# Kernel tuning notes

Hardware: AMD Instinct MI355X
Metric: run time of the kernel (lower is better)

Reference implementation:

```python
import jax, jax.numpy as jnp
import numpy as np

B, D, H, A, P, T = 65536, 256, 4, 32, 8, 32
TAU_MIN, TAU_MAX = 0.1, 5.0


def _ln(x, g, b, eps=1e-5):
    mu = jnp.mean(x, axis=-1, keepdims=True)
    v = jnp.mean((x - mu) ** 2, axis=-1, keepdims=True)
    return (x - mu) * jax.lax.rsqrt(v + eps) * g + b


def _bn(x, g, b, m, v, eps=1e-5):
    # eval-mode BatchNorm1d using running stats
    return (x - m) * jax.lax.rsqrt(v + eps) * g + b


def setup_inputs() -> dict:
    key = jax.random.key(0)
    ks = iter(jax.random.split(key, 64))
    rn = lambda shape, s: jax.random.normal(next(ks), shape, jnp.float32) * s
    un = lambda shape: jax.random.uniform(next(ks), shape, jnp.float32, 0.5, 1.5)
    z = lambda *shape: jnp.zeros(shape, jnp.float32)
    o = lambda *shape: jnp.ones(shape, jnp.float32)
    inp = {
        'x': jax.random.normal(next(ks), (B, D), jnp.float32),
        # input BatchNorm (eval mode)
        'bn0_g': o(D), 'bn0_b': z(D), 'bn0_m': rn((D,), 0.1), 'bn0_v': un((D,)),
        # per-head EDT params, stacked over H heads
        'qw': rn((H, D, A), 0.05), 'qb': z(H, A),
        'pk': rn((H, P, A), 0.02), 'pv': rn((H, P, A), 0.02),
        'tw1': rn((H, 1, T), 0.5), 'tb1': z(H, T),
        'tw2': rn((H, T, 1), 0.5), 'tb2': z(H, 1),
        'ow': rn((H, A, A), 0.1), 'ob': z(H, A),
        'lng': o(H, A), 'lnb': z(H, A),
        # head fusion
        'fp_w': rn((H * A, D), 0.05), 'fp_b': z(D),
        'fln_g': o(D), 'fln_b': z(D),
        # SE block
        'se_w1': rn((D, D // 4), 0.05), 'se_b1': z(D // 4),
        'se_w2': rn((D // 4, D), 0.05), 'se_b2': z(D),
        # hidden block 1: 256->256 (identity residual)
        'b1_w': rn((256, 256), 0.05), 'b1_b': z(256),
        'b1_g': o(256), 'b1_bb': z(256), 'b1_m': rn((256,), 0.1), 'b1_v': un((256,)),
        # hidden block 2: 256->128
        'b2_w': rn((256, 128), 0.05), 'b2_b': z(128),
        'b2_g': o(128), 'b2_bb': z(128), 'b2_m': rn((128,), 0.1), 'b2_v': un((128,)),
        'r2_w': rn((256, 128), 0.05), 'r2_b': z(128),
        # hidden block 3: 128->64
        'b3_w': rn((128, 64), 0.05), 'b3_b': z(64),
        'b3_g': o(64), 'b3_bb': z(64), 'b3_m': rn((64,), 0.1), 'b3_v': un((64,)),
        'r3_w': rn((128, 64), 0.05), 'r3_b': z(64),
        # classifier head
        'c1_w': rn((64, 32), 0.1), 'c1_b': z(32),
        'c2_w': rn((32, 1), 0.1), 'c2_b': z(1),
    }
    return inp


def reference(x, bn0_g, bn0_b, bn0_m, bn0_v, qw, qb, pk, pv, tw1, tb1, tw2, tb2,
              ow, ob, lng, lnb, fp_w, fp_b, fln_g, fln_b, se_w1, se_b1, se_w2, se_b2,
              b1_w, b1_b, b1_g, b1_bb, b1_m, b1_v,
              b2_w, b2_b, b2_g, b2_bb, b2_m, b2_v, r2_w, r2_b,
              b3_w, b3_b, b3_g, b3_bb, b3_m, b3_v, r3_w, r3_b,
              c1_w, c1_b, c2_w, c2_b):
    gelu = lambda t: jax.nn.gelu(t, approximate=False)
    xb = _bn(x, bn0_g, bn0_b, bn0_m, bn0_v)                      # (B, D)
    # ---- multi-head EDT prototype attention (vectorized over heads) ----
    q = jnp.einsum('bi,hia->bha', xb, qw) + qb                   # (B, H, A)
    logits = jnp.einsum('bha,hpa->bhp', q, pk) / jnp.sqrt(jnp.float32(A))
    lp = jax.nn.log_softmax(logits, axis=-1)                     # pass 1: entropy
    ent = -jnp.sum(jnp.exp(lp) * lp, axis=-1) / jnp.log(jnp.float32(P))  # (B, H)
    hid = jax.nn.relu(ent[..., None] * tw1[:, 0, :] + tb1)       # (B, H, T)
    tau = TAU_MIN + (TAU_MAX - TAU_MIN) * jax.nn.sigmoid(
        jnp.einsum('bht,ht->bh', hid, tw2[:, :, 0]) + tb2[:, 0])  # (B, H)
    attn = jax.nn.softmax(logits / tau[..., None], axis=-1)      # pass 2: tempered
    ho = jnp.einsum('bhp,hpa->bha', attn, pv)
    ho = jnp.einsum('bha,hae->bhe', ho, ow) + ob
    ho = _ln(ho, lng, lnb)                                       # per-head LayerNorm
    comb = ho.reshape(ho.shape[0], H * A)                        # concat heads
    att = _ln(comb @ fp_w + fp_b + xb, fln_g, fln_b)             # fuse + residual
    # ---- SE gating ----
    se = jax.nn.sigmoid(jax.nn.relu(att @ se_w1 + se_b1) @ se_w2 + se_b2)
    h = att * se
    # ---- residual MLP stack (Dropout inactive at eval) ----
    h = gelu(_bn(h @ b1_w + b1_b, b1_g, b1_bb, b1_m, b1_v)) + h
    h = gelu(_bn(h @ b2_w + b2_b, b2_g, b2_bb, b2_m, b2_v)) + (h @ r2_w + r2_b)
    h = gelu(_bn(h @ b3_w + b3_b, b3_g, b3_bb, b3_m, b3_v)) + (h @ r3_w + r3_b)
    # ---- classifier head ----
    return jax.nn.sigmoid(gelu(h @ c1_w + c1_b) @ c2_w + c2_b)   # (B, 1)
```

## Files before the change

### kernel.cpp

```cpp
#include <hip/hip_runtime.h>
#include <math.h>


typedef unsigned short u16;
typedef __attribute__((ext_vector_type(8))) short short8;
typedef __attribute__((ext_vector_type(4))) short short4v;
typedef __attribute__((ext_vector_type(4))) float f32x4;

struct Ptrs { const float* p[51]; };

__device__ __host__ __forceinline__ u16 f2bf(float f) {
  union { float f; unsigned int i; } v; v.f = f;
  unsigned int u = v.i;
  unsigned int r = (u + 0x7fffu + ((u >> 16) & 1u)) >> 16;
  return (u16)r;
}
__device__ __forceinline__ float bf2f(u16 u) {
  union { unsigned int i; float f; } v; v.i = ((unsigned int)u) << 16; return v.f;
}
__device__ __forceinline__ float gelu_exact(float y) {
  return 0.5f * y * (1.f + erff(y * 0.70710678118654752f));
}
__device__ __forceinline__ float sigmoidf_(float y) {
  return 1.f / (1.f + expf(-y));
}

#define QWT_O   0
#define FPT_O   32768
#define SE1T_O  65536
#define SE2T_O  81920
#define B1T_O   98304
#define B2T_O   163840
#define R2T_O   196608
#define B3T_O   229376
#define R3T_O   237568
#define C1T_O   245760
#define W_TOTAL 247808
#define WSP_F_OFF 123904
#define BN0S_P 0
#define BN0T_P 256
#define PK_P   512
#define PV_P   1536
#define OW_P   2560
#define TW1_P  6656
#define TB1_P  6784
#define TW2_P  6912
#define TB2_P  7040
#define OB_P   7044
#define LNG_P  7172
#define LNB_P  7300
#define QB_P   7428
#define FPB_P  7556
#define FLNG_P 7812
#define FLNB_P 8068
#define SEB1_P 8324
#define SEB2_P 8388
#define B1S_P  8644
#define B1TT_P 8900
#define B2S_P  9156
#define B2TT_P 9284
#define R2B_P  9412
#define B3S_P  9540
#define B3TT_P 9604
#define R3B_P  9668
#define C1B_P  9732
#define C2W_P  9764
#define C2B_P  9796
#define P_TOTAL 9797

#define XSTRIDE 264

__global__ void prep_weights(Ptrs P, u16* __restrict__ w) {
  for (int idx = blockIdx.x * blockDim.x + threadIdx.x; idx < W_TOTAL;
       idx += gridDim.x * blockDim.x) {
    int i = idx; float v;
    if (i < 32768)       { int n = i >> 8, k = i & 255; v = P.p[5][(n >> 5) * 8192 + k * 32 + (n & 31)]; }
    else if (i < 65536)  { i -= 32768;  int n = i >> 7, k = i & 127; v = P.p[17][k * 256 + n]; }
    else if (i < 81920)  { i -= 65536;  int n = i >> 8, k = i & 255; v = P.p[21][k * 64 + n]; }
    else if (i < 98304)  { i -= 81920;  int n = i >> 6, k = i & 63;  v = P.p[23][k * 256 + n]; }
    else if (i < 163840) { i -= 98304;  int n = i >> 8, k = i & 255; v = P.p[25][k * 256 + n]; }
    else if (i < 196608) { i -= 163840; int n = i >> 8, k = i & 255; v = P.p[31][k * 128 + n]; }
    else if (i < 229376) { i -= 196608; int n = i >> 8, k = i & 255; v = P.p[37][k * 128 + n]; }
    else if (i < 237568) { i -= 229376; int n = i >> 7, k = i & 127; v = P.p[39][k * 64 + n]; }
    else if (i < 245760) { i -= 237568; int n = i >> 7, k = i & 127; v = P.p[45][k * 64 + n]; }
    else                 { i -= 245760; int n = i >> 6, k = i & 63;  v = P.p[47][k * 32 + n]; }
    w[idx] = f2bf(v);
  }
}

__global__ void prep_params(Ptrs P, float* __restrict__ wp) {
  int idx = blockIdx.x * blockDim.x + threadIdx.x;
  if (idx >= P_TOTAL) return;
  const float eps = 1e-5f;
  int i = idx; float v;
  if (i < 256)        { v = P.p[1][i] * rsqrtf(P.p[4][i] + eps); }
  else if (i < 512)   { int c = i - 256; float s = P.p[1][c] * rsqrtf(P.p[4][c] + eps); v = P.p[2][c] - P.p[3][c] * s; }
  else if (i < 1536)  v = P.p[7][i - 512];
  else if (i < 2560)  v = P.p[8][i - 1536];
  else if (i < 6656)  v = P.p[13][i - 2560];
  else if (i < 6784)  v = P.p[9][i - 6656];
  else if (i < 6912)  v = P.p[10][i - 6784];
  else if (i < 7040)  v = P.p[11][i - 6912];
  else if (i < 7044)  v = P.p[12][i - 7040];
  else if (i < 7172)  v = P.p[14][i - 7044];
  else if (i < 7300)  v = P.p[15][i - 7172];
  else if (i < 7428)  v = P.p[16][i - 7300];
  else if (i < 7556)  v = P.p[6][i - 7428];
  else if (i < 7812)  v = P.p[18][i - 7556];
  else if (i < 8068)  v = P.p[19][i - 7812];
  else if (i < 8324)  v = P.p[20][i - 8068];
  else if (i < 8388)  v = P.p[22][i - 8324];
  else if (i < 8644)  v = P.p[24][i - 8388];
  else if (i < 8900)  { int c = i - 8644; v = P.p[27][c] * rsqrtf(P.p[30][c] + eps); }
  else if (i < 9156)  { int c = i - 8900; float s = P.p[27][c] * rsqrtf(P.p[30][c] + eps); v = P.p[28][c] + (P.p[26][c] - P.p[29][c]) * s; }
  else if (i < 9284)  { int c = i - 9156; v = P.p[33][c] * rsqrtf(P.p[36][c] + eps); }
  else if (i < 9412)  { int c = i - 9284; float s = P.p[33][c] * rsqrtf(P.p[36][c] + eps); v = P.p[34][c] + (P.p[32][c] - P.p[35][c]) * s; }
  else if (i < 9540)  v = P.p[38][i - 9412];
  else if (i < 9604)  { int c = i - 9540; v = P.p[41][c] * rsqrtf(P.p[44][c] + eps); }
  else if (i < 9668)  { int c = i - 9604; float s = P.p[41][c] * rsqrtf(P.p[44][c] + eps); v = P.p[42][c] + (P.p[40][c] - P.p[43][c]) * s; }
  else if (i < 9732)  v = P.p[46][i - 9668];
  else if (i < 9764)  v = P.p[48][i - 9732];
  else if (i < 9796)  v = P.p[49][i - 9764];
  else                v = P.p[50][0];
  wp[idx] = v;
}

template<int K, int NT>
__device__ __forceinline__ void gemm_tile(const u16* A, const u16* __restrict__ WT,
                                          int n0, int kg, int l15, f32x4 acc[4][NT]) {
#pragma unroll
  for (int kc = 0; kc < K / 32; ++kc) {
    short8 b[NT];
#pragma unroll
    for (int nt = 0; nt < NT; ++nt)
      b[nt] = *reinterpret_cast<const short8*>(WT + (n0 + nt * 16 + l15) * K + kc * 32 + kg * 8);
#pragma unroll
    for (int m = 0; m < 4; ++m) {
      short8 a = *reinterpret_cast<const short8*>(A + (m * 16 + l15) * XSTRIDE + kc * 32 + kg * 8);
#pragma unroll
      for (int nt = 0; nt < NT; ++nt)
        acc[m][nt] = __builtin_amdgcn_mfma_f32_16x16x32_bf16(a, b[nt], acc[m][nt], 0, 0, 0);
    }
  }
}

#define ZERO_ACC(acc, NT)                                         \
  _Pragma("unroll") for (int m_ = 0; m_ < 4; ++m_)                \
  _Pragma("unroll") for (int n_ = 0; n_ < NT; ++n_)               \
    acc[m_][n_] = (f32x4){0.f, 0.f, 0.f, 0.f};

__global__ __launch_bounds__(256) void fused_kernel(const float* __restrict__ x,
                                                    const u16* __restrict__ W,
                                                    const float* __restrict__ Pg,
                                                    float* __restrict__ out) {
  __shared__ __align__(16) u16 XA[64 * XSTRIDE];
  __shared__ __align__(16) u16 XB[64 * XSTRIDE];
  __shared__ __align__(16) float PRM[9800];

  const int tid = threadIdx.x;
  const int row0 = blockIdx.x * 64;
  const int wv = tid >> 6, lane = tid & 63;
  const int kg = lane >> 4, l15 = lane & 15;

  {
    const float4* src = reinterpret_cast<const float4*>(Pg);
    float4* dst = reinterpret_cast<float4*>(PRM);
    for (int i = tid; i < 2450; i += 256) dst[i] = src[i];
  }
  {
    const float4* x4 = reinterpret_cast<const float4*>(x);
    const float4* s4 = reinterpret_cast<const float4*>(Pg + BN0S_P);
    const float4* t4 = reinterpret_cast<const float4*>(Pg + BN0T_P);
    for (int it = tid; it < 4096; it += 256) {
      int r = it >> 6, c4 = it & 63;
      float4 v = x4[(size_t)(row0 + r) * 64 + c4];
      float4 s = s4[c4];
      float4 t = t4[c4];
      short4v o;
      o[0] = (short)f2bf(v.x * s.x + t.x);
      o[1] = (short)f2bf(v.y * s.y + t.y);
      o[2] = (short)f2bf(v.z * s.z + t.z);
      o[3] = (short)f2bf(v.w * s.w + t.w);
      *reinterpret_cast<short4v*>(&XA[r * XSTRIDE + c4 * 4]) = o;
    }
  }
  __syncthreads();

  {
    f32x4 acc[4][2];
    ZERO_ACC(acc, 2)
    gemm_tile<256, 2>(XA, W + QWT_O, wv * 32, kg, l15, acc);
#pragma unroll
    for (int m = 0; m < 4; ++m)
#pragma unroll
      for (int nt = 0; nt < 2; ++nt)
#pragma unroll
        for (int i = 0; i < 4; ++i) {
          int col = wv * 32 + nt * 16 + l15;
          int row = m * 16 + kg * 4 + i;
          XB[row * XSTRIDE + col] = f2bf(acc[m][nt][i] + PRM[QB_P + col]);
        }
  }
  __syncthreads();

  {
    const int h = wv;
    const int r = lane;
    float qv[32];
#pragma unroll
    for (int j = 0; j < 4; ++j) {
      short8 s = *reinterpret_cast<const short8*>(&XB[r * XSTRIDE + h * 32 + j * 8]);
#pragma unroll
      for (int e = 0; e < 8; ++e) qv[j * 8 + e] = bf2f((u16)s[e]);
    }
    float lp[8];
#pragma unroll
    for (int p = 0; p < 8; ++p) {
      float a = 0.f;
#pragma unroll
      for (int aa = 0; aa < 32; ++aa) a += qv[aa] * PRM[PK_P + h * 256 + p * 32 + aa];
      lp[p] = a * 0.17677669529663687f;
    }
    float mx = lp[0];
#pragma unroll
    for (int p = 1; p < 8; ++p) mx = fmaxf(mx, lp[p]);
    float se = 0.f;
#pragma unroll
    for (int p = 0; p < 8; ++p) se += expf(lp[p] - mx);
    float lse = mx + logf(se);
    float ent = 0.f;
#pragma unroll
    for (int p = 0; p < 8; ++p) { float t = lp[p] - lse; ent += expf(t) * t; }
    ent = -ent * 0.48089834696298783f;
    float sacc = 0.f;
#pragma unroll
    for (int t = 0; t < 32; ++t) {
      float hd = fmaxf(ent * PRM[TW1_P + h * 32 + t] + PRM[TB1_P + h * 32 + t], 0.f);
      sacc += hd * PRM[TW2_P + h * 32 + t];
    }
    float tau = 0.1f + 4.9f * sigmoidf_(sacc + PRM[TB2_P + h]);
    float itau = 1.f / tau;
    float at[8]; float s2 = 0.f;
#pragma unroll
    for (int p = 0; p < 8; ++p) { at[p] = expf((lp[p] - mx) * itau); s2 += at[p]; }
    float is2 = 1.f / s2;
    float ho[32];
#pragma unroll
    for (int aa = 0; aa < 32; ++aa) {
      float a = 0.f;
#pragma unroll
      for (int p = 0; p < 8; ++p) a += at[p] * PRM[PV_P + h * 256 + p * 32 + aa];
      ho[aa] = a * is2;
    }
    float h2[32]; float mu = 0.f;
#pragma unroll
    for (int e = 0; e < 32; ++e) {
      float a = PRM[OB_P + h * 32 + e];
#pragma unroll
      for (int aa = 0; aa < 32; ++aa) a += ho[aa] * PRM[OW_P + h * 1024 + aa * 32 + e];
      h2[e] = a; mu += a;
    }
    mu *= 0.03125f;
    float var = 0.f;
#pragma unroll
    for (int e = 0; e < 32; ++e) { float d = h2[e] - mu; var += d * d; }
    var *= 0.03125f;
    float rs = rsqrtf(var + 1e-5f);
#pragma unroll
    for (int e = 0; e < 32; ++e) {
      float v = (h2[e] - mu) * rs * PRM[LNG_P + h * 32 + e] + PRM[LNB_P + h * 32 + e];
      XB[r * XSTRIDE + h * 32 + e] = f2bf(v);
    }
  }
  __syncthreads();

  {
    f32x4 acc[4][4];
    ZERO_ACC(acc, 4)
    gemm_tile<128, 4>(XB, W + FPT_O, wv * 64, kg, l15, acc);
#pragma unroll
    for (int m = 0; m < 4; ++m)
#pragma unroll
      for (int nt = 0; nt < 4; ++nt)
#pragma unroll
        for (int i = 0; i < 4; ++i) {
          int col = wv * 64 + nt * 16 + l15;
          int row = m * 16 + kg * 4 + i;
          float v = acc[m][nt][i] + PRM[FPB_P + col] + bf2f(XA[row * XSTRIDE + col]);
          XA[row * XSTRIDE + col] = f2bf(v);
        }
  }
  __syncthreads();
  {
    int r = tid >> 2, qd = tid & 3;
    int base = r * XSTRIDE + qd * 64;
    float s = 0.f, s2 = 0.f;
#pragma unroll
    for (int j = 0; j < 8; ++j) {
      short8 v = *reinterpret_cast<const short8*>(&XA[base + j * 8]);
#pragma unroll
      for (int e = 0; e < 8; ++e) { float f = bf2f((u16)v[e]); s += f; s2 += f * f; }
    }
    s += __shfl_xor(s, 1);  s += __shfl_xor(s, 2);
    s2 += __shfl_xor(s2, 1); s2 += __shfl_xor(s2, 2);
    float mu = s * (1.f / 256.f);
    float var = s2 * (1.f / 256.f) - mu * mu;
    float rs = rsqrtf(var + 1e-5f);
#pragma unroll
    for (int j = 0; j < 8; ++j) {
      short8 v = *reinterpret_cast<const short8*>(&XA[base + j * 8]);
      short8 o;
#pragma unroll
      for (int e = 0; e < 8; ++e) {
        int col = qd * 64 + j * 8 + e;
        float f = (bf2f((u16)v[e]) - mu) * rs * PRM[FLNG_P + col] + PRM[FLNB_P + col];
        o[e] = (short)f2bf(f);
      }
      *reinterpret_cast<short8*>(&XA[base + j * 8]) = o;
    }
  }
  __syncthreads();

  {
    f32x4 acc[4][1];
    ZERO_ACC(acc, 1)
    gemm_tile<256, 1>(XA, W + SE1T_O, wv * 16, kg, l15, acc);
#pragma unroll
    for (int m = 0; m < 4; ++m)
#pragma unroll
      for (int i = 0; i < 4; ++i) {
        int col = wv * 16 + l15;
        int row = m * 16 + kg * 4 + i;
        XB[row * XSTRIDE + col] = f2bf(fmaxf(acc[m][0][i] + PRM[SEB1_P + col], 0.f));
      }
  }
  __syncthreads();

  {
    f32x4 acc[4][4];
    ZERO_ACC(acc, 4)
    gemm_tile<64, 4>(XB, W + SE2T_O, wv * 64, kg, l15, acc);
#pragma unroll
    for (int m = 0; m < 4; ++m)
#pragma unroll
      for (int nt = 0; nt < 4; ++nt)
#pragma unroll
        for (int i = 0; i < 4; ++i) {
          int col = wv * 64 + nt * 16 + l15;
          int row = m * 16 + kg * 4 + i;
          float g = sigmoidf_(acc[m][nt][i] + PRM[SEB2_P + col]);
          float a = bf2f(XA[row * XSTRIDE + col]);
          XA[row * XSTRIDE + col] = f2bf(a * g);
        }
  }
  __syncthreads();

  {
    f32x4 acc[4][4];
    ZERO_ACC(acc, 4)
    gemm_tile<256, 4>(XA, W + B1T_O, wv * 64, kg, l15, acc);
#pragma unroll
    for (int m = 0; m < 4; ++m)
#pragma unroll
      for (int nt = 0; nt < 4; ++nt)
#pragma unroll
        for (int i = 0; i < 4; ++i) {
          int col = wv * 64 + nt * 16 + l15;
          int row = m * 16 + kg * 4 + i;
          float y = PRM[B1S_P + col] * acc[m][nt][i] + PRM[B1TT_P + col];
          float g = gelu_exact(y);
          float h0 = bf2f(XA[row * XSTRIDE + col]);
          XB[row * XSTRIDE + col] = f2bf(g + h0);
        }
  }
  __syncthreads();

  {
    f32x4 acc[4][2], accr[4][2];
    ZERO_ACC(acc, 2)
    ZERO_ACC(accr, 2)
    gemm_tile<256, 2>(XB, W + B2T_O, wv * 32, kg, l15, acc);
    gemm_tile<256, 2>(XB, W + R2T_O, wv * 32, kg, l15, accr);
#pragma unroll
    for (int m = 0; m < 4; ++m)
#pragma unroll
      for (int nt = 0; nt < 2; ++nt)
#pragma unroll
        for (int i = 0; i < 4; ++i) {
          int col = wv * 32 + nt * 16 + l15;
          int row = m * 16 + kg * 4 + i;
          float y = PRM[B2S_P + col] * acc[m][nt][i] + PRM[B2TT_P + col];
          float g = gelu_exact(y);
          float y2 = accr[m][nt][i] + PRM[R2B_P + col];
          XA[row * XSTRIDE + col] = f2bf(g + y2);
        }
  }
  __syncthreads();

  {
    f32x4 acc[4][1], accr[4][1];
    ZERO_ACC(acc, 1)
    ZERO_ACC(accr, 1)
    gemm_tile<128, 1>(XA, W + B3T_O, wv * 16, kg, l15, acc);
    gemm_tile<128, 1>(XA, W + R3T_O, wv * 16, kg, l15, accr);
#pragma unroll
    for (int m = 0; m < 4; ++m)
#pragma unroll
      for (int i = 0; i < 4; ++i) {
        int col = wv * 16 + l15;
        int row = m * 16 + kg * 4 + i;
        float y = PRM[B3S_P + col] * acc[m][0][i] + PRM[B3TT_P + col];
        float g = gelu_exact(y);
        float y2 = accr[m][0][i] + PRM[R3B_P + col];
        XB[row * XSTRIDE + col] = f2bf(g + y2);
      }
  }
  __syncthreads();

  {
    f32x4 ac[2];
    ac[0] = (f32x4){0.f, 0.f, 0.f, 0.f};
    ac[1] = (f32x4){0.f, 0.f, 0.f, 0.f};
#pragma unroll
    for (int kc = 0; kc < 2; ++kc) {
      short8 b0 = *reinterpret_cast<const short8*>(W + C1T_O + (0 * 16 + l15) * 64 + kc * 32 + kg * 8);
      short8 b1 = *reinterpret_cast<const short8*>(W + C1T_O + (1 * 16 + l15) * 64 + kc * 32 + kg * 8);
      short8 a = *reinterpret_cast<const short8*>(&XB[(wv * 16 + l15) * XSTRIDE + kc * 32 + kg * 8]);
      ac[0] = __builtin_amdgcn_mfma_f32_16x16x32_bf16(a, b0, ac[0], 0, 0, 0);
      ac[1] = __builtin_amdgcn_mfma_f32_16x16x32_bf16(a, b1, ac[1], 0, 0, 0);
    }
#pragma unroll
    for (int nt = 0; nt < 2; ++nt)
#pragma unroll
      for (int i = 0; i < 4; ++i) {
        int col = nt * 16 + l15;
        int row = wv * 16 + kg * 4 + i;
        float y = ac[nt][i] + PRM[C1B_P + col];
        XB[row * XSTRIDE + 64 + col] = f2bf(gelu_exact(y));
      }
  }
  __syncthreads();

  if (tid < 64) {
    int r = tid;
    float s = PRM[C2B_P];
#pragma unroll
    for (int j = 0; j < 32; ++j) s += bf2f(XB[r * XSTRIDE + 64 + j]) * PRM[C2W_P + j];
    out[row0 + r] = sigmoidf_(s);
  }
}

extern "C" void kernel_launch(void* const* d_in, const int* in_sizes, int n_in,
                              void* d_out, int out_size, void* d_ws, size_t ws_size,
                              hipStream_t stream) {
  (void)in_sizes; (void)n_in; (void)out_size; (void)ws_size;
  Ptrs P;
  for (int i = 0; i < 51; ++i) P.p[i] = (const float*)d_in[i];

  u16* wsW = (u16*)d_ws;
  float* wsP = (float*)d_ws + WSP_F_OFF;

  prep_weights<<<256, 256, 0, stream>>>(P, wsW);
  prep_params<<<39, 256, 0, stream>>>(P, wsP);
  fused_kernel<<<1024, 256, 0, stream>>>((const float*)d_in[0], wsW, wsP, (float*)d_out);
}
```

Measured before the change: 425.9 us.

## Halve rows per block and read params from global instead of LDS

Each block now processes 32 rows instead of 64, and the grid doubles to match. The 39KB per-block copy of the parameter table into shared memory is removed, and parameters are read directly from global memory (cached). This cuts LDS use from about 107KB to 34KB and accumulator registers, so more blocks can be resident per CU and the per-block parameter copy goes away. In exchange, weight reuse per block is halved, the attention stage leaves half the lanes idle, and scalar parameter loads now go through the cache.

```diff
diff --git a/kernel.cpp b/kernel.cpp
--- a/kernel.cpp
+++ b/kernel.cpp
@@ -69,6 +69,7 @@
 #define P_TOTAL 9797
 
 #define XSTRIDE 264
+#define ROWS 32
 
 __global__ void prep_weights(Ptrs P, u16* __restrict__ w) {
   for (int idx = blockIdx.x * blockDim.x + threadIdx.x; idx < W_TOTAL;
@@ -127,7 +128,7 @@
 
 template<int K, int NT>
 __device__ __forceinline__ void gemm_tile(const u16* A, const u16* __restrict__ WT,
-                                          int n0, int kg, int l15, f32x4 acc[4][NT]) {
+                                          int n0, int kg, int l15, f32x4 acc[2][NT]) {
 #pragma unroll
   for (int kc = 0; kc < K / 32; ++kc) {
     short8 b[NT];
@@ -135,7 +136,7 @@
     for (int nt = 0; nt < NT; ++nt)
       b[nt] = *reinterpret_cast<const short8*>(WT + (n0 + nt * 16 + l15) * K + kc * 32 + kg * 8);
 #pragma unroll
-    for (int m = 0; m < 4; ++m) {
+    for (int m = 0; m < 2; ++m) {
       short8 a = *reinterpret_cast<const short8*>(A + (m * 16 + l15) * XSTRIDE + kc * 32 + kg * 8);
 #pragma unroll
       for (int nt = 0; nt < NT; ++nt)
@@ -145,33 +146,28 @@
 }
 
 #define ZERO_ACC(acc, NT)                                         \
-  _Pragma("unroll") for (int m_ = 0; m_ < 4; ++m_)                \
+  _Pragma("unroll") for (int m_ = 0; m_ < 2; ++m_)                \
   _Pragma("unroll") for (int n_ = 0; n_ < NT; ++n_)               \
     acc[m_][n_] = (f32x4){0.f, 0.f, 0.f, 0.f};
 
-__global__ __launch_bounds__(256) void fused_kernel(const float* __restrict__ x,
-                                                    const u16* __restrict__ W,
-                                                    const float* __restrict__ Pg,
-                                                    float* __restrict__ out) {
-  __shared__ __align__(16) u16 XA[64 * XSTRIDE];
-  __shared__ __align__(16) u16 XB[64 * XSTRIDE];
-  __shared__ __align__(16) float PRM[9800];
+__global__ __launch_bounds__(256, 4) void fused_kernel(const float* __restrict__ x,
+                                                       const u16* __restrict__ W,
+                                                       const float* __restrict__ Pg,
+                                                       float* __restrict__ out) {
+  __shared__ __align__(16) u16 XA[ROWS * XSTRIDE];
+  __shared__ __align__(16) u16 XB[ROWS * XSTRIDE];
 
   const int tid = threadIdx.x;
-  const int row0 = blockIdx.x * 64;
+  const int row0 = blockIdx.x * ROWS;
   const int wv = tid >> 6, lane = tid & 63;
   const int kg = lane >> 4, l15 = lane & 15;
 
-  {
-    const float4* src = reinterpret_cast<const float4*>(Pg);
-    float4* dst = reinterpret_cast<float4*>(PRM);
-    for (int i = tid; i < 2450; i += 256) dst[i] = src[i];
-  }
   {
     const float4* x4 = reinterpret_cast<const float4*>(x);
     const float4* s4 = reinterpret_cast<const float4*>(Pg + BN0S_P);
     const float4* t4 = reinterpret_cast<const float4*>(Pg + BN0T_P);
-    for (int it = tid; it < 4096; it += 256) {
+#pragma unroll
+    for (int it = tid; it < ROWS * 64; it += 256) {
       int r = it >> 6, c4 = it & 63;
       float4 v = x4[(size_t)(row0 + r) * 64 + c4];
       float4 s = s4[c4];
@@ -187,23 +183,23 @@
   __syncthreads();
 
   {
-    f32x4 acc[4][2];
+    f32x4 acc[2][2];
     ZERO_ACC(acc, 2)
     gemm_tile<256, 2>(XA, W + QWT_O, wv * 32, kg, l15, acc);
 #pragma unroll
-    for (int m = 0; m < 4; ++m)
+    for (int m = 0; m < 2; ++m)
 #pragma unroll
       for (int nt = 0; nt < 2; ++nt)
 #pragma unroll
         for (int i = 0; i < 4; ++i) {
           int col = wv * 32 + nt * 16 + l15;
           int row = m * 16 + kg * 4 + i;
-          XB[row * XSTRIDE + col] = f2bf(acc[m][nt][i] + PRM[QB_P + col]);
+          XB[row * XSTRIDE + col] = f2bf(acc[m][nt][i] + Pg[QB_P + col]);
         }
   }
   __syncthreads();
 
-  {
+  if (lane < ROWS) {
     const int h = wv;
     const int r = lane;
     float qv[32];
@@ -218,7 +214,7 @@
     for (int p = 0; p < 8; ++p) {
       float a = 0.f;
 #pragma unroll
-      for (int aa = 0; aa < 32; ++aa) a += qv[aa] * PRM[PK_P + h * 256 + p * 32 + aa];
+      for (int aa = 0; aa < 32; ++aa) a += qv[aa] * Pg[PK_P + h * 256 + p * 32 + aa];
       lp[p] = a * 0.17677669529663687f;
     }
     float mx = lp[0];
@@ -235,10 +231,10 @@
     float sacc = 0.f;
 #pragma unroll
     for (int t = 0; t < 32; ++t) {
-      float hd = fmaxf(ent * PRM[TW1_P + h * 32 + t] + PRM[TB1_P + h * 32 + t], 0.f);
-      sacc += hd * PRM[TW2_P + h * 32 + t];
-    }
-    float tau = 0.1f + 4.9f * sigmoidf_(sacc + PRM[TB2_P + h]);
+      float hd = fmaxf(ent * Pg[TW1_P + h * 32 + t] + Pg[TB1_P + h * 32 + t], 0.f);
+      sacc += hd * Pg[TW2_P + h * 32 + t];
+    }
+    float tau = 0.1f + 4.9f * sigmoidf_(sacc + Pg[TB2_P + h]);
     float itau = 1.f / tau;
     float at[8]; float s2 = 0.f;
 #pragma unroll
@@ -249,15 +245,15 @@
     for (int aa = 0; aa < 32; ++aa) {
       float a = 0.f;
 #pragma unroll
-      for (int p = 0; p < 8; ++p) a += at[p] * PRM[PV_P + h * 256 + p * 32 + aa];
+      for (int p = 0; p < 8; ++p) a += at[p] * Pg[PV_P + h * 256 + p * 32 + aa];
       ho[aa] = a * is2;
     }
     float h2[32]; float mu = 0.f;
 #pragma unroll
     for (int e = 0; e < 32; ++e) {
-      float a = PRM[OB_P + h * 32 + e];
-#pragma unroll
-      for (int aa = 0; aa < 32; ++aa) a += ho[aa] * PRM[OW_P + h * 1024 + aa * 32 + e];
+      float a = Pg[OB_P + h * 32 + e];
+#pragma unroll
+      for (int aa = 0; aa < 32; ++aa) a += ho[aa] * Pg[OW_P + h * 1024 + aa * 32 + e];
       h2[e] = a; mu += a;
     }
     mu *= 0.03125f;
@@ -268,52 +264,52 @@
     float rs = rsqrtf(var + 1e-5f);
 #pragma unroll
     for (int e = 0; e < 32; ++e) {
-      float v = (h2[e] - mu) * rs * PRM[LNG_P + h * 32 + e] + PRM[LNB_P + h * 32 + e];
+      float v = (h2[e] - mu) * rs * Pg[LNG_P + h * 32 + e] + Pg[LNB_P + h * 32 + e];
       XB[r * XSTRIDE + h * 32 + e] = f2bf(v);
     }
   }
   __syncthreads();
 
   {
-    f32x4 acc[4][4];
+    f32x4 acc[2][4];
     ZERO_ACC(acc, 4)
     gemm_tile<128, 4>(XB, W + FPT_O, wv * 64, kg, l15, acc);
 #pragma unroll
-    for (int m = 0; m < 4; ++m)
+    for (int m = 0; m < 2; ++m)
 #pragma unroll
       for (int nt = 0; nt < 4; ++nt)
 #pragma unroll
         for (int i = 0; i < 4; ++i) {
           int col = wv * 64 + nt * 16 + l15;
           int row = m * 16 + kg * 4 + i;
-          float v = acc[m][nt][i] + PRM[FPB_P + col] + bf2f(XA[row * XSTRIDE + col]);
+          float v = acc[m][nt][i] + Pg[FPB_P + col] + bf2f(XA[row * XSTRIDE + col]);
           XA[row * XSTRIDE + col] = f2bf(v);
         }
   }
   __syncthreads();
   {
-    int r = tid >> 2, qd = tid & 3;
-    int base = r * XSTRIDE + qd * 64;
+    int r = tid >> 3, oct = tid & 7;
+    int base = r * XSTRIDE + oct * 32;
     float s = 0.f, s2 = 0.f;
 #pragma unroll
-    for (int j = 0; j < 8; ++j) {
+    for (int j = 0; j < 4; ++j) {
       short8 v = *reinterpret_cast<const short8*>(&XA[base + j * 8]);
 #pragma unroll
       for (int e = 0; e < 8; ++e) { float f = bf2f((u16)v[e]); s += f; s2 += f * f; }
     }
-    s += __shfl_xor(s, 1);  s += __shfl_xor(s, 2);
-    s2 += __shfl_xor(s2, 1); s2 += __shfl_xor(s2, 2);
+    s += __shfl_xor(s, 1);  s += __shfl_xor(s, 2);  s += __shfl_xor(s, 4);
+    s2 += __shfl_xor(s2, 1); s2 += __shfl_xor(s2, 2); s2 += __shfl_xor(s2, 4);
     float mu = s * (1.f / 256.f);
     float var = s2 * (1.f / 256.f) - mu * mu;
     float rs = rsqrtf(var + 1e-5f);
 #pragma unroll
-    for (int j = 0; j < 8; ++j) {
+    for (int j = 0; j < 4; ++j) {
       short8 v = *reinterpret_cast<const short8*>(&XA[base + j * 8]);
       short8 o;
 #pragma unroll
       for (int e = 0; e < 8; ++e) {
-        int col = qd * 64 + j * 8 + e;
-        float f = (bf2f((u16)v[e]) - mu) * rs * PRM[FLNG_P + col] + PRM[FLNB_P + col];
+        int col = oct * 32 + j * 8 + e;
+        float f = (bf2f((u16)v[e]) - mu) * rs * Pg[FLNG_P + col] + Pg[FLNB_P + col];
         o[e] = (short)f2bf(f);
       }
       *reinterpret_cast<short8*>(&XA[base + j * 8]) = o;
@@ -322,33 +318,33 @@
   __syncthreads();
 
   {
-    f32x4 acc[4][1];
+    f32x4 acc[2][1];
     ZERO_ACC(acc, 1)
     gemm_tile<256, 1>(XA, W + SE1T_O, wv * 16, kg, l15, acc);
 #pragma unroll
-    for (int m = 0; m < 4; ++m)
+    for (int m = 0; m < 2; ++m)
 #pragma unroll
       for (int i = 0; i < 4; ++i) {
         int col = wv * 16 + l15;
         int row = m * 16 + kg * 4 + i;
-        XB[row * XSTRIDE + col] = f2bf(fmaxf(acc[m][0][i] + PRM[SEB1_P + col], 0.f));
+        XB[row * XSTRIDE + col] = f2bf(fmaxf(acc[m][0][i] + Pg[SEB1_P + col], 0.f));
       }
   }
   __syncthreads();
 
   {
-    f32x4 acc[4][4];
+    f32x4 acc[2][4];
     ZERO_ACC(acc, 4)
     gemm_tile<64, 4>(XB, W + SE2T_O, wv * 64, kg, l15, acc);
 #pragma unroll
-    for (int m = 0; m < 4; ++m)
+    for (int m = 0; m < 2; ++m)
 #pragma unroll
       for (int nt = 0; nt < 4; ++nt)
 #pragma unroll
         for (int i = 0; i < 4; ++i) {
           int col = wv * 64 + nt * 16 + l15;
           int row = m * 16 + kg * 4 + i;
-          float g = sigmoidf_(acc[m][nt][i] + PRM[SEB2_P + col]);
+          float g = sigmoidf_(acc[m][nt][i] + Pg[SEB2_P + col]);
           float a = bf2f(XA[row * XSTRIDE + col]);
           XA[row * XSTRIDE + col] = f2bf(a * g);
         }
@@ -356,18 +352,18 @@
   __syncthreads();
 
   {
-    f32x4 acc[4][4];
+    f32x4 acc[2][4];
     ZERO_ACC(acc, 4)
     gemm_tile<256, 4>(XA, W + B1T_O, wv * 64, kg, l15, acc);
 #pragma unroll
-    for (int m = 0; m < 4; ++m)
+    for (int m = 0; m < 2; ++m)
 #pragma unroll
       for (int nt = 0; nt < 4; ++nt)
 #pragma unroll
         for (int i = 0; i < 4; ++i) {
           int col = wv * 64 + nt * 16 + l15;
           int row = m * 16 + kg * 4 + i;
-          float y = PRM[B1S_P + col] * acc[m][nt][i] + PRM[B1TT_P + col];
+          float y = Pg[B1S_P + col] * acc[m][nt][i] + Pg[B1TT_P + col];
           float g = gelu_exact(y);
           float h0 = bf2f(XA[row * XSTRIDE + col]);
           XB[row * XSTRIDE + col] = f2bf(g + h0);
@@ -376,76 +372,71 @@
   __syncthreads();
 
   {
-    f32x4 acc[4][2], accr[4][2];
+    f32x4 acc[2][2], accr[2][2];
     ZERO_ACC(acc, 2)
     ZERO_ACC(accr, 2)
     gemm_tile<256, 2>(XB, W + B2T_O, wv * 32, kg, l15, acc);
     gemm_tile<256, 2>(XB, W + R2T_O, wv * 32, kg, l15, accr);
 #pragma unroll
-    for (int m = 0; m < 4; ++m)
+    for (int m = 0; m < 2; ++m)
 #pragma unroll
       for (int nt = 0; nt < 2; ++nt)
 #pragma unroll
         for (int i = 0; i < 4; ++i) {
           int col = wv * 32 + nt * 16 + l15;
           int row = m * 16 + kg * 4 + i;
-          float y = PRM[B2S_P + col] * acc[m][nt][i] + PRM[B2TT_P + col];
+          float y = Pg[B2S_P + col] * acc[m][nt][i] + Pg[B2TT_P + col];
           float g = gelu_exact(y);
-          float y2 = accr[m][nt][i] + PRM[R2B_P + col];
+          float y2 = accr[m][nt][i] + Pg[R2B_P + col];
           XA[row * XSTRIDE + col] = f2bf(g + y2);
         }
   }
   __syncthreads();
 
   {
-    f32x4 acc[4][1], accr[4][1];
+    f32x4 acc[2][1], accr[2][1];
     ZERO_ACC(acc, 1)
     ZERO_ACC(accr, 1)
     gemm_tile<128, 1>(XA, W + B3T_O, wv * 16, kg, l15, acc);
     gemm_tile<128, 1>(XA, W + R3T_O, wv * 16, kg, l15, accr);
 #pragma unroll
-    for (int m = 0; m < 4; ++m)
+    for (int m = 0; m < 2; ++m)
 #pragma unroll
       for (int i = 0; i < 4; ++i) {
         int col = wv * 16 + l15;
         int row = m * 16 + kg * 4 + i;
-        float y = PRM[B3S_P + col] * acc[m][0][i] + PRM[B3TT_P + col];
+        float y = Pg[B3S_P + col] * acc[m][0][i] + Pg[B3TT_P + col];
         float g = gelu_exact(y);
-        float y2 = accr[m][0][i] + PRM[R3B_P + col];
+        float y2 = accr[m][0][i] + Pg[R3B_P + col];
         XB[row * XSTRIDE + col] = f2bf(g + y2);
       }
   }
   __syncthreads();
 
   {
-    f32x4 ac[2];
-    ac[0] = (f32x4){0.f, 0.f, 0.f, 0.f};
-    ac[1] = (f32x4){0.f, 0.f, 0.f, 0.f};
+    const int mh = wv >> 1, nh = wv & 1;
+    f32x4 ac = (f32x4){0.f, 0.f, 0.f, 0.f};
 #pragma unroll
     for (int kc = 0; kc < 2; ++kc) {
-      short8 b0 = *reinterpret_cast<const short8*>(W + C1T_O + (0 * 16 + l15) * 64 + kc * 32 + kg * 8);
-      short8 b1 = *reinterpret_cast<const short8*>(W + C1T_O + (1 * 16 + l15) * 64 + kc * 32 + kg * 8);
-      short8 a = *reinterpret_cast<const short8*>(&XB[(wv * 16 + l15) * XSTRIDE + kc * 32 + kg * 8]);
-      ac[0] = __builtin_amdgcn_mfma_f32_16x16x32_bf16(a, b0, ac[0], 0, 0, 0);
-      ac[1] = __builtin_amdgcn_mfma_f32_16x16x32_bf16(a, b1, ac[1], 0, 0, 0);
-    }
-#pragma unroll
-    for (int nt = 0; nt < 2; ++nt)
-#pragma unroll
-      for (int i = 0; i < 4; ++i) {
-        int col = nt * 16 + l15;
-        int row = wv * 16 + kg * 4 + i;
-        float y = ac[nt][i] + PRM[C1B_P + col];
-        XB[row * XSTRIDE + 64 + col] = f2bf(gelu_exact(y));
-      }
-  }
-  __syncthreads();
-
-  if (tid < 64) {
+      short8 b = *reinterpret_cast<const short8*>(W + C1T_O + (nh * 16 + l15) * 64 + kc * 32 + kg * 8);
+      short8 a = *reinterpret_cast<const short8*>(&XB[(mh * 16 + l15) * XSTRIDE + kc * 32 + kg * 8]);
+      ac = __builtin_amdgcn_mfma_f32_16x16x32_bf16(a, b, ac, 0, 0, 0);
+    }
+#pragma unroll
+    for (int i = 0; i < 4; ++i) {
+      int col = nh * 16 + l15;
+      int row = mh * 16 + kg * 4 + i;
+      float y = ac[i] + Pg[C1B_P + col];
+      XB[row * XSTRIDE + 64 + col] = f2bf(gelu_exact(y));
+    }
+  }
+  __syncthreads();
+
+  if (tid < ROWS) {
     int r = tid;
-    float s = PRM[C2B_P];
-#pragma unroll
-    for (int j = 0; j < 32; ++j) s += bf2f(XB[r * XSTRIDE + 64 + j]) * PRM[C2W_P + j];
+    float s = Pg[C2B_P];
+#pragma unroll
+    for (int j = 0; j < 32; ++j) s += bf2f(XB[r * XSTRIDE + 64 + j]) * Pg[C2W_P + j];
     out[row0 + r] = sigmoidf_(s);
   }
 }
@@ -462,5 +453,5 @@
 
   prep_weights<<<256, 256, 0, stream>>>(P, wsW);
   prep_params<<<39, 256, 0, stream>>>(P, wsP);
-  fused_kernel<<<1024, 256, 0, stream>>>((const float*)d_in[0], wsW, wsP, (float*)d_out);
-}
+  fused_kernel<<<65536 / ROWS, 256, 0, stream>>>((const float*)d_in[0], wsW, wsP, (float*)d_out);
+}
```

Result: slower. 550.4 us (+29.3%).
